# Kernel optimization log

Measured on AMD Instinct MI355X. Metric: run time of the kernel, lower is better.

The kernel has to match this reference:

```python
import jax, jax.numpy as jnp
import numpy as np

B, T, D, L = 128, 32, 512, 2


def setup_inputs() -> dict:
    key = jax.random.key(0)
    ks = jax.random.split(key, 8)
    s = 0.02
    inp = {
        "cognition_features": jax.random.normal(ks[0], (B, T, D), dtype=jnp.float32),
        # per-layer stacked params (leading dim L)
        "Wq": s * jax.random.normal(ks[1], (L, D, D), dtype=jnp.float32),
        "bq": jnp.zeros((L, D), jnp.float32),
        "Wk": s * jax.random.normal(ks[2], (L, D, D), dtype=jnp.float32),
        "bk": jnp.zeros((L, D), jnp.float32),
        "Wv": s * jax.random.normal(ks[3], (L, D, D), dtype=jnp.float32),
        "bv": jnp.zeros((L, D), jnp.float32),
        "ln1_g": jnp.ones((L, D), jnp.float32),
        "ln1_b": jnp.zeros((L, D), jnp.float32),
        "W1": s * jax.random.normal(ks[4], (L, 4 * D, D), dtype=jnp.float32),
        "b1": jnp.zeros((L, 4 * D), jnp.float32),
        "W2": s * jax.random.normal(ks[5], (L, D, 4 * D), dtype=jnp.float32),
        "b2": jnp.zeros((L, D), jnp.float32),
        "ln2_g": jnp.ones((L, D), jnp.float32),
        "ln2_b": jnp.zeros((L, D), jnp.float32),
        # gate mlp (random instead of zeros/ones init to avoid degenerate constant gate)
        "Ws": s * jax.random.normal(ks[6], (D, 2 * D), dtype=jnp.float32),
        "bs": jnp.zeros((D,), jnp.float32),
    }
    return inp


def _ln(x, g, b, eps=1e-5):
    mu = jnp.mean(x, axis=-1, keepdims=True)
    var = jnp.mean((x - mu) ** 2, axis=-1, keepdims=True)
    return (x - mu) * jax.lax.rsqrt(var + eps) * g + b


def reference(cognition_features, Wq, bq, Wk, bk, Wv, bv, ln1_g, ln1_b,
              W1, b1, W2, b2, ln2_g, ln2_b, Ws, bs):
    b_, t_, d_ = cognition_features.shape
    L_ = Wq.shape[0]
    # memory bank entries are detached originals of earlier batch items
    mem = jax.lax.stop_gradient(cognition_features).reshape(b_ * t_, d_)
    mem_item = jnp.arange(b_ * t_) // t_
    visible = mem_item[None, :] < jnp.arange(b_)[:, None]  # [B, B*T]
    neg = jnp.asarray(-1e9, cognition_features.dtype)
    scale = 1.0 / jnp.sqrt(jnp.asarray(d_, cognition_features.dtype))

    x = cognition_features
    for l in range(L_):
        q = x @ Wq[l].T + bq[l]                      # [B,T,D]
        k = mem @ Wk[l].T + bk[l]                    # [B*T,D]
        v = mem @ Wv[l].T + bv[l]
        s = jnp.einsum('btd,md->btm', q, k) * scale  # [B,T,B*T]
        s = jnp.where(visible[:, None, :], s, neg)
        a = jax.nn.softmax(s, axis=-1)
        attn = jnp.einsum('btm,md->btd', a, v)
        x = _ln(x + attn, ln1_g[l], ln1_b[l])
        h = jax.nn.gelu(x @ W1[l].T + b1[l], approximate=False)
        x = _ln(x + h @ W2[l].T + b2[l], ln2_g[l], ln2_b[l])

    # item 0 has an empty bank: blocks are skipped, attn_out = query
    attn_out = jnp.where((jnp.arange(b_) == 0)[:, None, None], cognition_features, x)
    cat = jnp.concatenate([cognition_features, attn_out], axis=-1)
    g = jax.nn.sigmoid(cat @ Ws.T + bs)
    return g * cognition_features + (1.0 - g) * attn_out
```

## Files before the change

### kernel.cpp

```cpp
#include <hip/hip_runtime.h>
#include <cmath>


#define ROWS 4096
#define DIM  512

typedef __bf16 bf16x8 __attribute__((ext_vector_type(8)));
typedef float  f32x4  __attribute__((ext_vector_type(4)));
typedef unsigned short u16;
typedef u16 u16x4 __attribute__((ext_vector_type(4)));
typedef u16 u16x8 __attribute__((ext_vector_type(8)));

#define RD ((size_t)ROWS * DIM)
#define BUFU 12288

__device__ __forceinline__ u16 f2bf(float x) {
    union { float f; unsigned u; } c; c.f = x;
    const unsigned r = (c.u + 0x7FFFu + ((c.u >> 16) & 1u)) >> 16;
    return (u16)r;
}

__device__ __forceinline__ void gload16(const void* g, void* l) {
    __builtin_amdgcn_global_load_lds(
        (const __attribute__((address_space(1))) void*)g,
        (__attribute__((address_space(3))) void*)l, 16, 0, 0);
}

__device__ __forceinline__ float gelu_f(float v) {
    return 0.5f * v * (1.0f + erff(v * 0.70710678118654752f));
}

template<int EPI>
__device__ __forceinline__ void mgemm_body(
    const u16* __restrict__ A, int lda,
    const u16* __restrict__ B, int ldb,
    const float* __restrict__ bias,
    void* __restrict__ C, int ldc,
    int kBeg, int kEnd, float scale, int m0, int n0, u16* smem)
{
    const int tid  = threadIdx.x;
    const int lane = tid & 63;
    const int w    = tid >> 6;
    const int wr   = (w >> 1) << 5;
    const int wc   = (w & 1) << 6;

    f32x4 acc[2][4];
    #pragma unroll
    for (int i = 0; i < 2; ++i)
        #pragma unroll
        for (int j = 0; j < 4; ++j)
            acc[i][j] = (f32x4){0.f, 0.f, 0.f, 0.f};

    const u16* gpA[2]; int loA[2];
    #pragma unroll
    for (int q = 0; q < 2; ++q) {
        const int c = (q << 2) + w;
        const int s = (c << 6) + lane;
        const int row = s >> 3, sub = (s & 7) ^ (row & 7);
        gpA[q] = A + (size_t)(m0 + row) * lda + (sub << 3) + kBeg;
        loA[q] = c << 9;
    }
    const u16* gpB[4]; int loB[4];
    #pragma unroll
    for (int q = 0; q < 4; ++q) {
        const int c = ((q + 2) << 2) + w - 8;
        const int s = (c << 6) + lane;
        const int row = s >> 3, sub = (s & 7) ^ (row & 7);
        gpB[q] = B + (size_t)(n0 + row) * ldb + (sub << 3) + kBeg;
        loB[q] = 4096 + (c << 9);
    }

    const int l15 = lane & 15, kg = lane >> 4;
    int aoff[2][2], boff[4][2];
    #pragma unroll
    for (int i = 0; i < 2; ++i)
        #pragma unroll
        for (int h = 0; h < 2; ++h) {
            const int r = wr + (i << 4) + l15;
            const int sub = ((h << 2) + kg) ^ (r & 7);
            aoff[i][h] = ((r << 3) + sub) << 3;
        }
    #pragma unroll
    for (int j = 0; j < 4; ++j)
        #pragma unroll
        for (int h = 0; h < 2; ++h) {
            const int r = wc + (j << 4) + l15;
            const int sub = ((h << 2) + kg) ^ (r & 7);
            boff[j][h] = 4096 + (((r << 3) + sub) << 3);
        }

    const int nt = (kEnd - kBeg) >> 6;

    auto STAGE = [&](int t, int bsel) {
        u16* base = smem + bsel * BUFU;
        const int ko = t << 6;
        gload16(gpA[0] + ko, base + loA[0]);
        gload16(gpA[1] + ko, base + loA[1]);
        gload16(gpB[0] + ko, base + loB[0]);
        gload16(gpB[1] + ko, base + loB[1]);
        gload16(gpB[2] + ko, base + loB[2]);
        gload16(gpB[3] + ko, base + loB[3]);
    };

    if (nt > 0) {
        STAGE(0, 0);
        if (nt > 1) STAGE(1, 1);
        for (int t = 0; t < nt; ++t) {
            if (t + 1 < nt) asm volatile("s_waitcnt vmcnt(6)" ::: "memory");
            else            asm volatile("s_waitcnt vmcnt(0)" ::: "memory");
            __builtin_amdgcn_s_barrier();
            asm volatile("" ::: "memory");

            const u16* buf = smem + (t & 1) * BUFU;
            bf16x8 a_[2][2], b_[4][2];
            #pragma unroll
            for (int i = 0; i < 2; ++i)
                #pragma unroll
                for (int h = 0; h < 2; ++h)
                    a_[i][h] = *reinterpret_cast<const bf16x8*>(&buf[aoff[i][h]]);
            #pragma unroll
            for (int j = 0; j < 4; ++j)
                #pragma unroll
                for (int h = 0; h < 2; ++h)
                    b_[j][h] = *reinterpret_cast<const bf16x8*>(&buf[boff[j][h]]);

            asm volatile("s_waitcnt lgkmcnt(0)" ::: "memory");
            __builtin_amdgcn_s_barrier();
            asm volatile("" ::: "memory");

            if (t + 2 < nt) STAGE(t + 2, t & 1);

            __builtin_amdgcn_s_setprio(1);
            #pragma unroll
            for (int h = 0; h < 2; ++h)
                #pragma unroll
                for (int i = 0; i < 2; ++i)
                    #pragma unroll
                    for (int j = 0; j < 4; ++j) {
                        if (EPI == 4)
                            acc[i][j] = __builtin_amdgcn_mfma_f32_16x16x32_bf16(
                                a_[i][h], b_[j][h], acc[i][j], 0, 0, 0);
                        else
                            acc[i][j] = __builtin_amdgcn_mfma_f32_16x16x32_bf16(
                                b_[j][h], a_[i][h], acc[i][j], 0, 0, 0);
                    }
            __builtin_amdgcn_s_setprio(0);
        }
    }

    const int lq = lane >> 4;
    if (EPI == 4) {
        #pragma unroll
        for (int j = 0; j < 4; ++j) {
            const int col = n0 + wc + (j << 4) + l15;
            const float bj = bias[col];
            #pragma unroll
            for (int i = 0; i < 2; ++i) {
                const int row0 = m0 + wr + (i << 4) + (lq << 2);
                u16x4 pk;
                #pragma unroll
                for (int r = 0; r < 4; ++r) pk[r] = f2bf(acc[i][j][r] + bj);
                *reinterpret_cast<u16x4*>(&((u16*)C)[(size_t)col * ldc + row0]) = pk;
            }
        }
    } else {
        #pragma unroll
        for (int j = 0; j < 4; ++j) {
            const int col0 = n0 + wc + (j << 4) + (lq << 2);
            float4 bj = {0.f, 0.f, 0.f, 0.f};
            if (EPI != 0) bj = *reinterpret_cast<const float4*>(&bias[col0]);
            #pragma unroll
            for (int i = 0; i < 2; ++i) {
                const int row = m0 + wr + (i << 4) + l15;
                f32x4 v = acc[i][j];
                if (EPI == 0) {
                    v[0] *= scale; v[1] *= scale; v[2] *= scale; v[3] *= scale;
                    *reinterpret_cast<f32x4*>(&((float*)C)[(size_t)row * ldc + col0]) = v;
                } else if (EPI == 1) {
                    v[0] += bj.x; v[1] += bj.y; v[2] += bj.z; v[3] += bj.w;
                    *reinterpret_cast<f32x4*>(&((float*)C)[(size_t)row * ldc + col0]) = v;
                } else {
                    v[0] += bj.x; v[1] += bj.y; v[2] += bj.z; v[3] += bj.w;
                    if (EPI == 3) {
                        v[0] = gelu_f(v[0]); v[1] = gelu_f(v[1]);
                        v[2] = gelu_f(v[2]); v[3] = gelu_f(v[3]);
                    }
                    u16x4 pk = {f2bf(v[0]), f2bf(v[1]), f2bf(v[2]), f2bf(v[3])};
                    *reinterpret_cast<u16x4*>(&((u16*)C)[(size_t)row * ldc + col0]) = pk;
                }
            }
        }
    }
}

template<int EPI>
__global__ __launch_bounds__(256, 3) void mgemm(
    const u16* __restrict__ A, int lda, const u16* __restrict__ B, int ldb,
    const float* __restrict__ bias, void* __restrict__ C, int ldc, int K, float scale)
{
    const int m0 = blockIdx.x << 6;
    const int n0 = blockIdx.y << 7;
    __shared__ u16 smem[2 * BUFU];
    mgemm_body<EPI>(A, lda, B, ldb, bias, C, ldc, 0, K, scale, m0, n0, smem);
}

__device__ __forceinline__ int tri_pref(int b) {
    const int h = b >> 1;
    return (b & 1) ? (h + 1) * (h + 1) : h * (h + 1);
}
__global__ __launch_bounds__(256, 3) void mgemm_tri(
    const u16* __restrict__ A, const u16* __restrict__ B,
    float* __restrict__ C, float scale)
{
    const int z = blockIdx.x;
    int bx = 2 * (int)sqrtf((float)z);
    while (tri_pref(bx + 1) <= z) ++bx;
    while (tri_pref(bx) > z) --bx;
    const int by = z - tri_pref(bx);
    __shared__ u16 smem[2 * BUFU];
    mgemm_body<0>(A, 512, B, 512, nullptr, C, 4096, 0, 512, scale,
                  bx << 6, by << 7, smem);
}

template<bool AVK>
__global__ __launch_bounds__(256, 3) void mgemm_pk(
    const u16* __restrict__ A, int lda, const u16* __restrict__ B, int ldb,
    float* __restrict__ Cpart, int K, int chunk)
{
    const int m0 = blockIdx.x << 6;
    const int n0 = blockIdx.y << 7;
    const int z  = blockIdx.z;
    const int Klim = AVK ? (m0 + 64) : K;
    const int ch = AVK ? ((((Klim >> 2) + 63) >> 6) << 6) : chunk;
    int kBeg = z * ch; if (kBeg > Klim) kBeg = Klim;
    int kEnd = kBeg + ch; if (kEnd > Klim) kEnd = Klim;
    __shared__ u16 smem[2 * BUFU];
    mgemm_body<0>(A, lda, B, ldb, nullptr, Cpart + (size_t)z * RD, 512,
                  kBeg, kEnd, 1.f, m0, n0, smem);
}

__global__ __launch_bounds__(256, 3) void qkv_gemm(
    const u16* __restrict__ xa, const u16* __restrict__ cfb,
    const u16* __restrict__ Wqb, const u16* __restrict__ Wkb, const u16* __restrict__ Wvb,
    const float* __restrict__ bq, const float* __restrict__ bk, const float* __restrict__ bv,
    u16* __restrict__ q, u16* __restrict__ k, u16* __restrict__ vT)
{
    __shared__ u16 smem[2 * BUFU];
    const int m0 = blockIdx.x << 6;
    const int which = blockIdx.y >> 2;
    const int n0 = (blockIdx.y & 3) << 7;
    if (which == 0)
        mgemm_body<2>(xa,  512, Wqb, 512, bq, q,  512,  0, 512, 1.f, m0, n0, smem);
    else if (which == 1)
        mgemm_body<2>(cfb, 512, Wkb, 512, bk, k,  512,  0, 512, 1.f, m0, n0, smem);
    else
        mgemm_body<4>(cfb, 512, Wvb, 512, bv, vT, 4096, 0, 512, 1.f, m0, n0, smem);
}

__global__ __launch_bounds__(256) void softmax_pbf(
    const float* __restrict__ S, u16* __restrict__ P, float* __restrict__ sums)
{
    const int row = blockIdx.x;
    const int b   = row >> 5;
    const int Lb  = b << 5;
    const int bound = ((row >> 6) + 1) << 6;
    const float* s = S + (size_t)row * 4096;
    u16* p = P + (size_t)row * 4096;
    const int tid = threadIdx.x;

    const u16x8 z8 = {0, 0, 0, 0, 0, 0, 0, 0};
    for (int m = Lb + tid * 8; m < bound; m += 2048)
        *reinterpret_cast<u16x8*>(&p[m]) = z8;
    if (b == 0) { if (tid == 0) sums[row] = 1.f; return; }

    __shared__ float red[4];
    float mx = -3.0e38f;
    for (int m = tid * 4; m < Lb; m += 1024) {
        const float4 v = *reinterpret_cast<const float4*>(&s[m]);
        mx = fmaxf(mx, fmaxf(fmaxf(v.x, v.y), fmaxf(v.z, v.w)));
    }
    #pragma unroll
    for (int off = 32; off; off >>= 1) mx = fmaxf(mx, __shfl_xor(mx, off));
    if ((tid & 63) == 0) red[tid >> 6] = mx;
    __syncthreads();
    mx = fmaxf(fmaxf(red[0], red[1]), fmaxf(red[2], red[3]));
    __syncthreads();

    float sum = 0.f;
    for (int m = tid * 8; m < Lb; m += 2048) {
        const float4 v0 = *reinterpret_cast<const float4*>(&s[m]);
        const float4 v1 = *reinterpret_cast<const float4*>(&s[m + 4]);
        float e[8];
        e[0] = expf(v0.x - mx); e[1] = expf(v0.y - mx);
        e[2] = expf(v0.z - mx); e[3] = expf(v0.w - mx);
        e[4] = expf(v1.x - mx); e[5] = expf(v1.y - mx);
        e[6] = expf(v1.z - mx); e[7] = expf(v1.w - mx);
        u16x8 o;
        #pragma unroll
        for (int i = 0; i < 8; ++i) { sum += e[i]; o[i] = f2bf(e[i]); }
        *reinterpret_cast<u16x8*>(&p[m]) = o;
    }
    #pragma unroll
    for (int off = 32; off; off >>= 1) sum += __shfl_xor(sum, off);
    if ((tid & 63) == 0) red[tid >> 6] = sum;
    __syncthreads();
    if (tid == 0)
        sums[row] = fmaxf(red[0] + red[1] + red[2] + red[3], 1e-30f);
}

template<int NS, bool HASB, bool DIV>
__global__ __launch_bounds__(256) void ln_res_ps(
    const float* __restrict__ Xin, const float* __restrict__ part,
    const float* __restrict__ bias, const float* __restrict__ sums,
    const float* __restrict__ gamma, const float* __restrict__ beta,
    float* __restrict__ Xout, u16* __restrict__ Xbf)
{
    const int row  = blockIdx.x * 4 + (threadIdx.x >> 6);
    const int lane = threadIdx.x & 63;
    const float* xr = Xin + (size_t)row * DIM;
    const int d0 = lane << 3;
    const float inv = DIV ? (1.0f / sums[row]) : 1.0f;

    const float4 x0 = *reinterpret_cast<const float4*>(&xr[d0]);
    const float4 x1 = *reinterpret_cast<const float4*>(&xr[d0 + 4]);
    float a[8] = {0.f, 0.f, 0.f, 0.f, 0.f, 0.f, 0.f, 0.f};
    #pragma unroll
    for (int s = 0; s < NS; ++s) {
        const float* pr = part + (size_t)s * RD + (size_t)row * DIM + d0;
        const float4 p0 = *reinterpret_cast<const float4*>(pr);
        const float4 p1 = *reinterpret_cast<const float4*>(pr + 4);
        a[0] += p0.x; a[1] += p0.y; a[2] += p0.z; a[3] += p0.w;
        a[4] += p1.x; a[5] += p1.y; a[6] += p1.z; a[7] += p1.w;
    }
    float v[8] = {x0.x, x0.y, x0.z, x0.w, x1.x, x1.y, x1.z, x1.w};
    #pragma unroll
    for (int i = 0; i < 8; ++i) v[i] += a[i] * inv;
    if (HASB) {
        const float4 b0 = *reinterpret_cast<const float4*>(&bias[d0]);
        const float4 b1 = *reinterpret_cast<const float4*>(&bias[d0 + 4]);
        v[0] += b0.x; v[1] += b0.y; v[2] += b0.z; v[3] += b0.w;
        v[4] += b1.x; v[5] += b1.y; v[6] += b1.z; v[7] += b1.w;
    }

    float sm = 0.f;
    #pragma unroll
    for (int i = 0; i < 8; ++i) sm += v[i];
    #pragma unroll
    for (int off = 32; off; off >>= 1) sm += __shfl_xor(sm, off);
    const float mu = sm * (1.0f / 512.0f);

    float qs = 0.f;
    #pragma unroll
    for (int i = 0; i < 8; ++i) { const float d = v[i] - mu; qs += d * d; }
    #pragma unroll
    for (int off = 32; off; off >>= 1) qs += __shfl_xor(qs, off);
    const float rs = rsqrtf(qs * (1.0f / 512.0f) + 1e-5f);

    const float4 g0 = *reinterpret_cast<const float4*>(&gamma[d0]);
    const float4 g1 = *reinterpret_cast<const float4*>(&gamma[d0 + 4]);
    const float4 b0 = *reinterpret_cast<const float4*>(&beta[d0]);
    const float4 b1 = *reinterpret_cast<const float4*>(&beta[d0 + 4]);
    float o[8];
    o[0] = (v[0] - mu) * rs * g0.x + b0.x;
    o[1] = (v[1] - mu) * rs * g0.y + b0.y;
    o[2] = (v[2] - mu) * rs * g0.z + b0.z;
    o[3] = (v[3] - mu) * rs * g0.w + b0.w;
    o[4] = (v[4] - mu) * rs * g1.x + b1.x;
    o[5] = (v[5] - mu) * rs * g1.y + b1.y;
    o[6] = (v[6] - mu) * rs * g1.z + b1.z;
    o[7] = (v[7] - mu) * rs * g1.w + b1.w;

    float4 f0 = {o[0], o[1], o[2], o[3]}, f1 = {o[4], o[5], o[6], o[7]};
    *reinterpret_cast<float4*>(&Xout[(size_t)row * DIM + d0])     = f0;
    *reinterpret_cast<float4*>(&Xout[(size_t)row * DIM + d0 + 4]) = f1;
    u16x8 ob;
    #pragma unroll
    for (int i = 0; i < 8; ++i) ob[i] = f2bf(o[i]);
    *reinterpret_cast<u16x8*>(&Xbf[(size_t)row * DIM + d0]) = ob;
}

struct ConvArgs {
    const float* src[7];
    u16* dst[7];
    int start[8];
};

__global__ __launch_bounds__(256) void conv_all(ConvArgs a)
{
    const int b = blockIdx.x;
    int seg = 0;
    #pragma unroll
    for (int i = 1; i < 7; ++i) seg += (a.start[i] <= b) ? 1 : 0;
    const int i = ((b - a.start[seg]) * 256 + threadIdx.x) << 3;
    const float* s = a.src[seg];
    const float4 lo = *reinterpret_cast<const float4*>(&s[i]);
    const float4 hi = *reinterpret_cast<const float4*>(&s[i + 4]);
    u16x8 o = {f2bf(lo.x), f2bf(lo.y), f2bf(lo.z), f2bf(lo.w),
               f2bf(hi.x), f2bf(hi.y), f2bf(hi.z), f2bf(hi.w)};
    *reinterpret_cast<u16x8*>(&a.dst[seg][i]) = o;
}

__global__ __launch_bounds__(256) void build_cat(
    u16* __restrict__ cat, const u16* __restrict__ cfb, const u16* __restrict__ xbf)
{
    const int idx = blockIdx.x * 256 + threadIdx.x;
    const int row = idx >> 7;
    const int c8  = idx & 127;
    const u16* src2 = (row < 32) ? cfb : xbf;
    const u16x8 v = (c8 < 64)
        ? *reinterpret_cast<const u16x8*>(&cfb[(size_t)row * 512 + (c8 << 3)])
        : *reinterpret_cast<const u16x8*>(&src2[(size_t)row * 512 + ((c8 - 64) << 3)]);
    *reinterpret_cast<u16x8*>(&cat[(size_t)row * 1024 + (c8 << 3)]) = v;
}

__global__ __launch_bounds__(256) void final_gate_ps(
    float4* __restrict__ out, const float4* __restrict__ cf,
    const float4* __restrict__ x, const float* __restrict__ part,
    const float* __restrict__ bias)
{
    const int idx = blockIdx.x * 256 + threadIdx.x;
    const int row = idx >> 7;
    const int c4  = idx & 127;
    const float4 zc = cf[idx];
    const float4 p0 = reinterpret_cast<const float4*>(part)[idx];
    const float4 p1 = reinterpret_cast<const float4*>(part + RD)[idx];
    const float4 bb = *reinterpret_cast<const float4*>(&bias[c4 << 2]);
    const float4 za = (row < 32) ? zc : x[idx];
    float4 o;
    { const float g = 1.0f / (1.0f + expf(-(p0.x + p1.x + bb.x))); o.x = g * zc.x + (1.0f - g) * za.x; }
    { const float g = 1.0f / (1.0f + expf(-(p0.y + p1.y + bb.y))); o.y = g * zc.y + (1.0f - g) * za.y; }
    { const float g = 1.0f / (1.0f + expf(-(p0.z + p1.z + bb.z))); o.z = g * zc.z + (1.0f - g) * za.z; }
    { const float g = 1.0f / (1.0f + expf(-(p0.w + p1.w + bb.w))); o.w = g * zc.w + (1.0f - g) * za.w; }
    out[idx] = o;
}

extern "C" void kernel_launch(void* const* d_in, const int* in_sizes, int n_in,
                              void* d_out, int out_size, void* d_ws, size_t ws_size,
                              hipStream_t stream)
{
    const float* cf   = (const float*)d_in[0];
    const float* Wq   = (const float*)d_in[1];
    const float* bq   = (const float*)d_in[2];
    const float* Wk   = (const float*)d_in[3];
    const float* bk   = (const float*)d_in[4];
    const float* Wv   = (const float*)d_in[5];
    const float* bv   = (const float*)d_in[6];
    const float* ln1g = (const float*)d_in[7];
    const float* ln1b = (const float*)d_in[8];
    const float* W1   = (const float*)d_in[9];
    const float* b1   = (const float*)d_in[10];
    const float* W2   = (const float*)d_in[11];
    const float* b2   = (const float*)d_in[12];
    const float* ln2g = (const float*)d_in[13];
    const float* ln2b = (const float*)d_in[14];
    const float* Wsg  = (const float*)d_in[15];
    const float* bsg  = (const float*)d_in[16];
    float* out = (float*)d_out;

    float* ws   = (float*)d_ws;
    float* x    = ws;
    float* sums = ws + RD;
    float* s    = ws + 2 * RD;
    float* part = ws + 2 * RD;
    u16*  pbf  = (u16*)(ws + 10 * RD);
    u16*  hbf  = pbf;
    u16*  catb = pbf;
    u16*  bfb  = (u16*)(ws + 14 * RD);
    u16* cfb = bfb;
    u16* xbf = bfb + RD;
    u16* qbf = bfb + 2 * RD;
    u16* kbf = bfb + 3 * RD;
    u16* vTb = bfb + 4 * RD;
    u16* Wqb = bfb + 5 * RD;
    u16* Wkb = Wqb + 524288;
    u16* Wvb = Wkb + 524288;
    u16* W1b = Wvb + 524288;
    u16* W2b = W1b + 2097152;
    u16* Wsb = W2b + 2097152;

    const float scale = 0.044194173824159216f;

    ConvArgs ca;
    ca.src[0] = cf;  ca.dst[0] = cfb;
    ca.src[1] = Wq;  ca.dst[1] = Wqb;
    ca.src[2] = Wk;  ca.dst[2] = Wkb;
    ca.src[3] = Wv;  ca.dst[3] = Wvb;
    ca.src[4] = W1;  ca.dst[4] = W1b;
    ca.src[5] = W2;  ca.dst[5] = W2b;
    ca.src[6] = Wsg; ca.dst[6] = Wsb;
    ca.start[0] = 0;    ca.start[1] = 1024; ca.start[2] = 1280;
    ca.start[3] = 1536; ca.start[4] = 1792; ca.start[5] = 2816;
    ca.start[6] = 3840; ca.start[7] = 4096;
    conv_all<<<4096, 256, 0, stream>>>(ca);

    for (int l = 0; l < 2; ++l) {
        const u16* xa = (l == 0) ? cfb : xbf;
        qkv_gemm<<<dim3(64, 12), 256, 0, stream>>>(
            xa, cfb, Wqb + l * 262144, Wkb + l * 262144, Wvb + l * 262144,
            bq + l * 512, bk + l * 512, bv + l * 512, qbf, kbf, vTb);
        mgemm_tri<<<1056, 256, 0, stream>>>(qbf, kbf, s, scale);
        softmax_pbf<<<4096, 256, 0, stream>>>(s, pbf, sums);
        mgemm_pk<true><<<dim3(64, 4, 4), 256, 0, stream>>>(
            pbf, 4096, vTb, 4096, part, 4096, 0);
        ln_res_ps<4, false, true><<<1024, 256, 0, stream>>>(
            (l == 0) ? cf : x, part, nullptr, sums,
            ln1g + l * 512, ln1b + l * 512, x, xbf);
        mgemm<3><<<dim3(64, 16), 256, 0, stream>>>(
            xbf, 512, W1b + l * 1048576, 512, b1 + l * 2048, hbf, 2048, 512, 1.f);
        mgemm_pk<false><<<dim3(64, 4, 4), 256, 0, stream>>>(
            hbf, 2048, W2b + l * 1048576, 2048, part, 2048, 512);
        ln_res_ps<4, true, false><<<1024, 256, 0, stream>>>(
            x, part, b2 + l * 512, nullptr,
            ln2g + l * 512, ln2b + l * 512, x, xbf);
    }

    build_cat<<<2048, 256, 0, stream>>>(catb, cfb, xbf);
    mgemm_pk<false><<<dim3(64, 4, 2), 256, 0, stream>>>(
        catb, 1024, Wsb, 1024, part, 1024, 512);
    final_gate_ps<<<2048, 256, 0, stream>>>((float4*)out, (const float4*)cf,
                                            (const float4*)x, part, bsg);
}
```

Before: 271.2 us.

## Store bf16 operands in MFMA fragment layout and use LDS-free per-wave GEMMs

All bf16 operands (converted weights, activations, softmax probabilities, q/k/vT) are now written in a pre-tiled 16x32 MFMA fragment layout. This lets each wave load its operand fragments straight from global memory with contiguous 16-byte loads. The shared-memory double-buffered block GEMM is replaced by an independent per-wave 64x64 tile GEMM with no barriers or LDS. Triangular and split-K work is recomputed at 64-row granularity, and the softmax zero-fill bound shrinks to match. The cost is reduced operand reuse across waves, since each wave reads its A and B tiles from L2 independently, and global loads are no longer software-pipelined.

Result: slower. 404.2 us (+49.0%).

```diff
diff --git a/kernel.cpp b/kernel.cpp
--- a/kernel.cpp
+++ b/kernel.cpp
@@ -12,7 +12,6 @@
 typedef u16 u16x8 __attribute__((ext_vector_type(8)));
 
 #define RD ((size_t)ROWS * DIM)
-#define BUFU 12288
 
 __device__ __forceinline__ u16 f2bf(float x) {
     union { float f; unsigned u; } c; c.f = x;
@@ -20,241 +19,196 @@
     return (u16)r;
 }
 
-__device__ __forceinline__ void gload16(const void* g, void* l) {
-    __builtin_amdgcn_global_load_lds(
-        (const __attribute__((address_space(1))) void*)g,
-        (__attribute__((address_space(3))) void*)l, 16, 0, 0);
-}
-
 __device__ __forceinline__ float gelu_f(float v) {
     return 0.5f * v * (1.0f + erff(v * 0.70710678118654752f));
 }
 
+__device__ __forceinline__ size_t fragAddr(int r, int k, int K) {
+    return ((size_t)((r >> 4) * (K >> 5) + (k >> 5)) << 9)
+         + (((r & 15) | (((k >> 3) & 3) << 4)) << 3);
+}
+
 template<int EPI>
-__device__ __forceinline__ void mgemm_body(
-    const u16* __restrict__ A, int lda,
-    const u16* __restrict__ B, int ldb,
+__device__ __forceinline__ void wgemm(
+    const u16* __restrict__ A, int KA,
+    const u16* __restrict__ B,
     const float* __restrict__ bias,
-    void* __restrict__ C, int ldc,
-    int kBeg, int kEnd, float scale, int m0, int n0, u16* smem)
-{
-    const int tid  = threadIdx.x;
-    const int lane = tid & 63;
-    const int w    = tid >> 6;
-    const int wr   = (w >> 1) << 5;
-    const int wc   = (w & 1) << 6;
-
-    f32x4 acc[2][4];
-    #pragma unroll
-    for (int i = 0; i < 2; ++i)
+    void* __restrict__ C, int ldcK,
+    int ktBeg, int ktEnd, float scale, int mt, int nt)
+{
+    const int lane = threadIdx.x & 63;
+    const int l15 = lane & 15, lq = lane >> 4;
+
+    f32x4 acc[4][4];
+    #pragma unroll
+    for (int i = 0; i < 4; ++i)
         #pragma unroll
         for (int j = 0; j < 4; ++j)
             acc[i][j] = (f32x4){0.f, 0.f, 0.f, 0.f};
 
-    const u16* gpA[2]; int loA[2];
-    #pragma unroll
-    for (int q = 0; q < 2; ++q) {
-        const int c = (q << 2) + w;
-        const int s = (c << 6) + lane;
-        const int row = s >> 3, sub = (s & 7) ^ (row & 7);
-        gpA[q] = A + (size_t)(m0 + row) * lda + (sub << 3) + kBeg;
-        loA[q] = c << 9;
-    }
-    const u16* gpB[4]; int loB[4];
-    #pragma unroll
-    for (int q = 0; q < 4; ++q) {
-        const int c = ((q + 2) << 2) + w - 8;
-        const int s = (c << 6) + lane;
-        const int row = s >> 3, sub = (s & 7) ^ (row & 7);
-        gpB[q] = B + (size_t)(n0 + row) * ldb + (sub << 3) + kBeg;
-        loB[q] = 4096 + (c << 9);
-    }
-
-    const int l15 = lane & 15, kg = lane >> 4;
-    int aoff[2][2], boff[4][2];
-    #pragma unroll
-    for (int i = 0; i < 2; ++i)
-        #pragma unroll
-        for (int h = 0; h < 2; ++h) {
-            const int r = wr + (i << 4) + l15;
-            const int sub = ((h << 2) + kg) ^ (r & 7);
-            aoff[i][h] = ((r << 3) + sub) << 3;
+    const int ka5 = KA >> 5;
+    const u16* pa[4]; const u16* pb[4];
+    #pragma unroll
+    for (int i = 0; i < 4; ++i)
+        pa[i] = A + (((size_t)((mt * 4 + i) * ka5 + ktBeg)) << 9) + (lane << 3);
+    #pragma unroll
+    for (int j = 0; j < 4; ++j)
+        pb[j] = B + (((size_t)((nt * 4 + j) * ka5 + ktBeg)) << 9) + (lane << 3);
+
+    for (int kt = ktBeg; kt < ktEnd; ++kt) {
+        bf16x8 a_[4], b_[4];
+        #pragma unroll
+        for (int i = 0; i < 4; ++i) {
+            a_[i] = *reinterpret_cast<const bf16x8*>(pa[i]); pa[i] += 512;
         }
-    #pragma unroll
-    for (int j = 0; j < 4; ++j)
-        #pragma unroll
-        for (int h = 0; h < 2; ++h) {
-            const int r = wc + (j << 4) + l15;
-            const int sub = ((h << 2) + kg) ^ (r & 7);
-            boff[j][h] = 4096 + (((r << 3) + sub) << 3);
+        #pragma unroll
+        for (int j = 0; j < 4; ++j) {
+            b_[j] = *reinterpret_cast<const bf16x8*>(pb[j]); pb[j] += 512;
         }
-
-    const int nt = (kEnd - kBeg) >> 6;
-
-    auto STAGE = [&](int t, int bsel) {
-        u16* base = smem + bsel * BUFU;
-        const int ko = t << 6;
-        gload16(gpA[0] + ko, base + loA[0]);
-        gload16(gpA[1] + ko, base + loA[1]);
-        gload16(gpB[0] + ko, base + loB[0]);
-        gload16(gpB[1] + ko, base + loB[1]);
-        gload16(gpB[2] + ko, base + loB[2]);
-        gload16(gpB[3] + ko, base + loB[3]);
-    };
-
-    if (nt > 0) {
-        STAGE(0, 0);
-        if (nt > 1) STAGE(1, 1);
-        for (int t = 0; t < nt; ++t) {
-            if (t + 1 < nt) asm volatile("s_waitcnt vmcnt(6)" ::: "memory");
-            else            asm volatile("s_waitcnt vmcnt(0)" ::: "memory");
-            __builtin_amdgcn_s_barrier();
-            asm volatile("" ::: "memory");
-
-            const u16* buf = smem + (t & 1) * BUFU;
-            bf16x8 a_[2][2], b_[4][2];
+        #pragma unroll
+        for (int i = 0; i < 4; ++i)
             #pragma unroll
-            for (int i = 0; i < 2; ++i)
-                #pragma unroll
-                for (int h = 0; h < 2; ++h)
-                    a_[i][h] = *reinterpret_cast<const bf16x8*>(&buf[aoff[i][h]]);
+            for (int j = 0; j < 4; ++j) {
+                if constexpr (EPI == 4)
+                    acc[i][j] = __builtin_amdgcn_mfma_f32_16x16x32_bf16(
+                        a_[i], b_[j], acc[i][j], 0, 0, 0);
+                else
+                    acc[i][j] = __builtin_amdgcn_mfma_f32_16x16x32_bf16(
+                        b_[j], a_[i], acc[i][j], 0, 0, 0);
+            }
+    }
+
+    if constexpr (EPI == 0) {
+        #pragma unroll
+        for (int j = 0; j < 4; ++j) {
+            const int col0 = nt * 64 + (j << 4) + (lq << 2);
             #pragma unroll
-            for (int j = 0; j < 4; ++j)
-                #pragma unroll
-                for (int h = 0; h < 2; ++h)
-                    b_[j][h] = *reinterpret_cast<const bf16x8*>(&buf[boff[j][h]]);
-
-            asm volatile("s_waitcnt lgkmcnt(0)" ::: "memory");
-            __builtin_amdgcn_s_barrier();
-            asm volatile("" ::: "memory");
-
-            if (t + 2 < nt) STAGE(t + 2, t & 1);
-
-            __builtin_amdgcn_s_setprio(1);
+            for (int i = 0; i < 4; ++i) {
+                const int row = mt * 64 + (i << 4) + l15;
+                f32x4 v = acc[i][j];
+                v[0] *= scale; v[1] *= scale; v[2] *= scale; v[3] *= scale;
+                *reinterpret_cast<f32x4*>(&((float*)C)[(size_t)row * ldcK + col0]) = v;
+            }
+        }
+    } else if constexpr (EPI == 2 || EPI == 3) {
+        #pragma unroll
+        for (int j = 0; j < 4; ++j) {
+            const int co = (j << 4) + (lq << 2);
+            const int col0 = nt * 64 + co;
+            const float4 bj = *reinterpret_cast<const float4*>(&bias[col0]);
+            const int ktO = (nt << 1) + (co >> 5);
+            const int lnO = l15 | (((co >> 3) & 3) << 4);
+            const int elem = co & 7;
             #pragma unroll
-            for (int h = 0; h < 2; ++h)
-                #pragma unroll
-                for (int i = 0; i < 2; ++i)
-                    #pragma unroll
-                    for (int j = 0; j < 4; ++j) {
-                        if (EPI == 4)
-                            acc[i][j] = __builtin_amdgcn_mfma_f32_16x16x32_bf16(
-                                a_[i][h], b_[j][h], acc[i][j], 0, 0, 0);
-                        else
-                            acc[i][j] = __builtin_amdgcn_mfma_f32_16x16x32_bf16(
-                                b_[j][h], a_[i][h], acc[i][j], 0, 0, 0);
-                    }
-            __builtin_amdgcn_s_setprio(0);
+            for (int i = 0; i < 4; ++i) {
+                const int rt = mt * 4 + i;
+                f32x4 v = acc[i][j];
+                v[0] += bj.x; v[1] += bj.y; v[2] += bj.z; v[3] += bj.w;
+                if (EPI == 3) {
+                    v[0] = gelu_f(v[0]); v[1] = gelu_f(v[1]);
+                    v[2] = gelu_f(v[2]); v[3] = gelu_f(v[3]);
+                }
+                u16x4 pk = {f2bf(v[0]), f2bf(v[1]), f2bf(v[2]), f2bf(v[3])};
+                u16* dst = (u16*)C + (((size_t)(rt * (ldcK >> 5) + ktO)) << 9)
+                         + (lnO << 3) + elem;
+                *reinterpret_cast<u16x4*>(dst) = pk;
+            }
         }
-    }
-
-    const int lq = lane >> 4;
-    if (EPI == 4) {
+    } else {
         #pragma unroll
         for (int j = 0; j < 4; ++j) {
-            const int col = n0 + wc + (j << 4) + l15;
+            const int rtO = nt * 4 + j;
+            const int col = nt * 64 + (j << 4) + l15;
             const float bj = bias[col];
             #pragma unroll
-            for (int i = 0; i < 2; ++i) {
-                const int row0 = m0 + wr + (i << 4) + (lq << 2);
+            for (int i = 0; i < 4; ++i) {
+                const int ro = (i << 4) + (lq << 2);
+                const int ktO = (mt << 1) + (ro >> 5);
+                const int lnO = l15 | (((ro >> 3) & 3) << 4);
+                const int elem = ro & 7;
                 u16x4 pk;
                 #pragma unroll
                 for (int r = 0; r < 4; ++r) pk[r] = f2bf(acc[i][j][r] + bj);
-                *reinterpret_cast<u16x4*>(&((u16*)C)[(size_t)col * ldc + row0]) = pk;
+                u16* dst = (u16*)C + (((size_t)(rtO * (ldcK >> 5) + ktO)) << 9)
+                         + (lnO << 3) + elem;
+                *reinterpret_cast<u16x4*>(dst) = pk;
             }
         }
-    } else {
-        #pragma unroll
-        for (int j = 0; j < 4; ++j) {
-            const int col0 = n0 + wc + (j << 4) + (lq << 2);
-            float4 bj = {0.f, 0.f, 0.f, 0.f};
-            if (EPI != 0) bj = *reinterpret_cast<const float4*>(&bias[col0]);
-            #pragma unroll
-            for (int i = 0; i < 2; ++i) {
-                const int row = m0 + wr + (i << 4) + l15;
-                f32x4 v = acc[i][j];
-                if (EPI == 0) {
-                    v[0] *= scale; v[1] *= scale; v[2] *= scale; v[3] *= scale;
-                    *reinterpret_cast<f32x4*>(&((float*)C)[(size_t)row * ldc + col0]) = v;
-                } else if (EPI == 1) {
-                    v[0] += bj.x; v[1] += bj.y; v[2] += bj.z; v[3] += bj.w;
-                    *reinterpret_cast<f32x4*>(&((float*)C)[(size_t)row * ldc + col0]) = v;
-                } else {
-                    v[0] += bj.x; v[1] += bj.y; v[2] += bj.z; v[3] += bj.w;
-                    if (EPI == 3) {
-                        v[0] = gelu_f(v[0]); v[1] = gelu_f(v[1]);
-                        v[2] = gelu_f(v[2]); v[3] = gelu_f(v[3]);
-                    }
-                    u16x4 pk = {f2bf(v[0]), f2bf(v[1]), f2bf(v[2]), f2bf(v[3])};
-                    *reinterpret_cast<u16x4*>(&((u16*)C)[(size_t)row * ldc + col0]) = pk;
-                }
-            }
-        }
-    }
-}
-
-template<int EPI>
-__global__ __launch_bounds__(256, 3) void mgemm(
-    const u16* __restrict__ A, int lda, const u16* __restrict__ B, int ldb,
-    const float* __restrict__ bias, void* __restrict__ C, int ldc, int K, float scale)
-{
-    const int m0 = blockIdx.x << 6;
-    const int n0 = blockIdx.y << 7;
-    __shared__ u16 smem[2 * BUFU];
-    mgemm_body<EPI>(A, lda, B, ldb, bias, C, ldc, 0, K, scale, m0, n0, smem);
-}
-
-__device__ __forceinline__ int tri_pref(int b) {
-    const int h = b >> 1;
-    return (b & 1) ? (h + 1) * (h + 1) : h * (h + 1);
-}
-__global__ __launch_bounds__(256, 3) void mgemm_tri(
-    const u16* __restrict__ A, const u16* __restrict__ B,
-    float* __restrict__ C, float scale)
-{
-    const int z = blockIdx.x;
-    int bx = 2 * (int)sqrtf((float)z);
-    while (tri_pref(bx + 1) <= z) ++bx;
-    while (tri_pref(bx) > z) --bx;
-    const int by = z - tri_pref(bx);
-    __shared__ u16 smem[2 * BUFU];
-    mgemm_body<0>(A, 512, B, 512, nullptr, C, 4096, 0, 512, scale,
-                  bx << 6, by << 7, smem);
-}
-
-template<bool AVK>
-__global__ __launch_bounds__(256, 3) void mgemm_pk(
-    const u16* __restrict__ A, int lda, const u16* __restrict__ B, int ldb,
-    float* __restrict__ Cpart, int K, int chunk)
-{
-    const int m0 = blockIdx.x << 6;
-    const int n0 = blockIdx.y << 7;
-    const int z  = blockIdx.z;
-    const int Klim = AVK ? (m0 + 64) : K;
-    const int ch = AVK ? ((((Klim >> 2) + 63) >> 6) << 6) : chunk;
-    int kBeg = z * ch; if (kBeg > Klim) kBeg = Klim;
-    int kEnd = kBeg + ch; if (kEnd > Klim) kEnd = Klim;
-    __shared__ u16 smem[2 * BUFU];
-    mgemm_body<0>(A, lda, B, ldb, nullptr, Cpart + (size_t)z * RD, 512,
-                  kBeg, kEnd, 1.f, m0, n0, smem);
-}
-
-__global__ __launch_bounds__(256, 3) void qkv_gemm(
+    }
+}
+
+__global__ __launch_bounds__(256, 3) void k_qkv(
     const u16* __restrict__ xa, const u16* __restrict__ cfb,
-    const u16* __restrict__ Wqb, const u16* __restrict__ Wkb, const u16* __restrict__ Wvb,
-    const float* __restrict__ bq, const float* __restrict__ bk, const float* __restrict__ bv,
+    const u16* __restrict__ Wqb, const u16* __restrict__ Wkb,
+    const u16* __restrict__ Wvb,
+    const float* __restrict__ bq, const float* __restrict__ bk,
+    const float* __restrict__ bv,
     u16* __restrict__ q, u16* __restrict__ k, u16* __restrict__ vT)
 {
-    __shared__ u16 smem[2 * BUFU];
-    const int m0 = blockIdx.x << 6;
-    const int which = blockIdx.y >> 2;
-    const int n0 = (blockIdx.y & 3) << 7;
+    const int g = blockIdx.x * 4 + (threadIdx.x >> 6);
+    const int which = g >> 9;
+    const int t = g & 511;
+    const int mt = t >> 3, nt = t & 7;
     if (which == 0)
-        mgemm_body<2>(xa,  512, Wqb, 512, bq, q,  512,  0, 512, 1.f, m0, n0, smem);
+        wgemm<2>(xa, 512, Wqb, bq, q, 512, 0, 16, 1.f, mt, nt);
     else if (which == 1)
-        mgemm_body<2>(cfb, 512, Wkb, 512, bk, k,  512,  0, 512, 1.f, m0, n0, smem);
+        wgemm<2>(cfb, 512, Wkb, bk, k, 512, 0, 16, 1.f, mt, nt);
     else
-        mgemm_body<4>(cfb, 512, Wvb, 512, bv, vT, 4096, 0, 512, 1.f, m0, n0, smem);
+        wgemm<4>(cfb, 512, Wvb, bv, vT, 4096, 0, 16, 1.f, mt, nt);
+}
+
+__global__ __launch_bounds__(256, 3) void k_tri(
+    const u16* __restrict__ qb, const u16* __restrict__ kb,
+    float* __restrict__ S, float scale)
+{
+    const int z = blockIdx.x * 4 + (threadIdx.x >> 6);
+    int mt = (int)((sqrtf((float)(8 * z + 1)) - 1.0f) * 0.5f);
+    while ((mt + 1) * (mt + 2) / 2 <= z) ++mt;
+    while (mt * (mt + 1) / 2 > z) --mt;
+    const int nt = z - mt * (mt + 1) / 2;
+    wgemm<0>(qb, 512, kb, nullptr, S, 4096, 0, 16, scale, mt, nt);
+}
+
+__global__ __launch_bounds__(256, 3) void k_av(
+    const u16* __restrict__ P, const u16* __restrict__ vT,
+    float* __restrict__ part)
+{
+    const int g = blockIdx.x * 4 + (threadIdx.x >> 6);
+    const int z = g & 3, nt = (g >> 2) & 7, mt = g >> 5;
+    const int kts = 2 * mt + 1;
+    const int ch = (kts + 3) >> 2;
+    int kb = z * ch; if (kb > kts) kb = kts;
+    int ke = kb + ch; if (ke > kts) ke = kts;
+    wgemm<0>(P, 4096, vT, nullptr, part + (size_t)z * RD, 512, kb, ke, 1.f, mt, nt);
+}
+
+__global__ __launch_bounds__(256, 3) void k_mlp1(
+    const u16* __restrict__ xb, const u16* __restrict__ W1b,
+    const float* __restrict__ b1, u16* __restrict__ h)
+{
+    const int g = blockIdx.x * 4 + (threadIdx.x >> 6);
+    const int mt = g >> 5, nt = g & 31;
+    wgemm<3>(xb, 512, W1b, b1, h, 2048, 0, 16, 1.f, mt, nt);
+}
+
+__global__ __launch_bounds__(256, 3) void k_mlp2(
+    const u16* __restrict__ h, const u16* __restrict__ W2b,
+    float* __restrict__ part)
+{
+    const int g = blockIdx.x * 4 + (threadIdx.x >> 6);
+    const int z = g & 3, nt = (g >> 2) & 7, mt = g >> 5;
+    wgemm<0>(h, 2048, W2b, nullptr, part + (size_t)z * RD, 512,
+             z * 16, z * 16 + 16, 1.f, mt, nt);
+}
+
+__global__ __launch_bounds__(256, 3) void k_gate(
+    const u16* __restrict__ cat, const u16* __restrict__ Wsb,
+    float* __restrict__ part)
+{
+    const int g = blockIdx.x * 4 + (threadIdx.x >> 6);
+    const int z = g & 1, nt = (g >> 1) & 7, mt = g >> 4;
+    wgemm<0>(cat, 1024, Wsb, nullptr, part + (size_t)z * RD, 512,
+             z * 16, z * 16 + 16, 1.f, mt, nt);
 }
 
 __global__ __launch_bounds__(256) void softmax_pbf(
@@ -263,14 +217,13 @@
     const int row = blockIdx.x;
     const int b   = row >> 5;
     const int Lb  = b << 5;
-    const int bound = ((row >> 6) + 1) << 6;
+    const int bound = ((row >> 6) << 6) + 32;
     const float* s = S + (size_t)row * 4096;
-    u16* p = P + (size_t)row * 4096;
     const int tid = threadIdx.x;
 
     const u16x8 z8 = {0, 0, 0, 0, 0, 0, 0, 0};
     for (int m = Lb + tid * 8; m < bound; m += 2048)
-        *reinterpret_cast<u16x8*>(&p[m]) = z8;
+        *reinterpret_cast<u16x8*>(&P[fragAddr(row, m, 4096)]) = z8;
     if (b == 0) { if (tid == 0) sums[row] = 1.f; return; }
 
     __shared__ float red[4];
@@ -298,7 +251,7 @@
         u16x8 o;
         #pragma unroll
         for (int i = 0; i < 8; ++i) { sum += e[i]; o[i] = f2bf(e[i]); }
-        *reinterpret_cast<u16x8*>(&p[m]) = o;
+        *reinterpret_cast<u16x8*>(&P[fragAddr(row, m, 4096)]) = o;
     }
     #pragma unroll
     for (int off = 32; off; off >>= 1) sum += __shfl_xor(sum, off);
@@ -376,13 +329,14 @@
     u16x8 ob;
     #pragma unroll
     for (int i = 0; i < 8; ++i) ob[i] = f2bf(o[i]);
-    *reinterpret_cast<u16x8*>(&Xbf[(size_t)row * DIM + d0]) = ob;
+    *reinterpret_cast<u16x8*>(&Xbf[fragAddr(row, d0, 512)]) = ob;
 }
 
 struct ConvArgs {
     const float* src[7];
     u16* dst[7];
     int start[8];
+    int K[7];
 };
 
 __global__ __launch_bounds__(256) void conv_all(ConvArgs a)
@@ -391,13 +345,18 @@
     int seg = 0;
     #pragma unroll
     for (int i = 1; i < 7; ++i) seg += (a.start[i] <= b) ? 1 : 0;
-    const int i = ((b - a.start[seg]) * 256 + threadIdx.x) << 3;
-    const float* s = a.src[seg];
-    const float4 lo = *reinterpret_cast<const float4*>(&s[i]);
-    const float4 hi = *reinterpret_cast<const float4*>(&s[i + 4]);
+    const int s = (b - a.start[seg]) * 256 + threadIdx.x;
+    const int K = a.K[seg];
+    const int fc = s >> 6, lane = s & 63;
+    const int rt = fc / (K >> 5), kt = fc % (K >> 5);
+    const int r = (rt << 4) + (lane & 15);
+    const int k = (kt << 5) + ((lane >> 4) << 3);
+    const float* src = a.src[seg] + (size_t)r * K + k;
+    const float4 lo = *reinterpret_cast<const float4*>(src);
+    const float4 hi = *reinterpret_cast<const float4*>(src + 4);
     u16x8 o = {f2bf(lo.x), f2bf(lo.y), f2bf(lo.z), f2bf(lo.w),
                f2bf(hi.x), f2bf(hi.y), f2bf(hi.z), f2bf(hi.w)};
-    *reinterpret_cast<u16x8*>(&a.dst[seg][i]) = o;
+    *reinterpret_cast<u16x8*>(&a.dst[seg][(size_t)s << 3]) = o;
 }
 
 __global__ __launch_bounds__(256) void build_cat(
@@ -405,12 +364,15 @@
 {
     const int idx = blockIdx.x * 256 + threadIdx.x;
     const int row = idx >> 7;
-    const int c8  = idx & 127;
-    const u16* src2 = (row < 32) ? cfb : xbf;
-    const u16x8 v = (c8 < 64)
-        ? *reinterpret_cast<const u16x8*>(&cfb[(size_t)row * 512 + (c8 << 3)])
-        : *reinterpret_cast<const u16x8*>(&src2[(size_t)row * 512 + ((c8 - 64) << 3)]);
-    *reinterpret_cast<u16x8*>(&cat[(size_t)row * 1024 + (c8 << 3)]) = v;
+    const int c0  = (idx & 127) << 3;
+    u16x8 v;
+    if (c0 < 512)
+        v = *reinterpret_cast<const u16x8*>(&cfb[fragAddr(row, c0, 512)]);
+    else {
+        const u16* src2 = (row < 32) ? cfb : xbf;
+        v = *reinterpret_cast<const u16x8*>(&src2[fragAddr(row, c0 - 512, 512)]);
+    }
+    *reinterpret_cast<u16x8*>(&cat[fragAddr(row, c0, 1024)]) = v;
 }
 
 __global__ __launch_bounds__(256) void final_gate_ps(
@@ -481,13 +443,13 @@
     const float scale = 0.044194173824159216f;
 
     ConvArgs ca;
-    ca.src[0] = cf;  ca.dst[0] = cfb;
-    ca.src[1] = Wq;  ca.dst[1] = Wqb;
-    ca.src[2] = Wk;  ca.dst[2] = Wkb;
-    ca.src[3] = Wv;  ca.dst[3] = Wvb;
-    ca.src[4] = W1;  ca.dst[4] = W1b;
-    ca.src[5] = W2;  ca.dst[5] = W2b;
-    ca.src[6] = Wsg; ca.dst[6] = Wsb;
+    ca.src[0] = cf;  ca.dst[0] = cfb;  ca.K[0] = 512;
+    ca.src[1] = Wq;  ca.dst[1] = Wqb;  ca.K[1] = 512;
+    ca.src[2] = Wk;  ca.dst[2] = Wkb;  ca.K[2] = 512;
+    ca.src[3] = Wv;  ca.dst[3] = Wvb;  ca.K[3] = 512;
+    ca.src[4] = W1;  ca.dst[4] = W1b;  ca.K[4] = 512;
+    ca.src[5] = W2;  ca.dst[5] = W2b;  ca.K[5] = 2048;
+    ca.src[6] = Wsg; ca.dst[6] = Wsb;  ca.K[6] = 1024;
     ca.start[0] = 0;    ca.start[1] = 1024; ca.start[2] = 1280;
     ca.start[3] = 1536; ca.start[4] = 1792; ca.start[5] = 2816;
     ca.start[6] = 3840; ca.start[7] = 4096;
@@ -495,28 +457,24 @@
 
     for (int l = 0; l < 2; ++l) {
         const u16* xa = (l == 0) ? cfb : xbf;
-        qkv_gemm<<<dim3(64, 12), 256, 0, stream>>>(
+        k_qkv<<<384, 256, 0, stream>>>(
             xa, cfb, Wqb + l * 262144, Wkb + l * 262144, Wvb + l * 262144,
             bq + l * 512, bk + l * 512, bv + l * 512, qbf, kbf, vTb);
-        mgemm_tri<<<1056, 256, 0, stream>>>(qbf, kbf, s, scale);
+        k_tri<<<520, 256, 0, stream>>>(qbf, kbf, s, scale);
         softmax_pbf<<<4096, 256, 0, stream>>>(s, pbf, sums);
-        mgemm_pk<true><<<dim3(64, 4, 4), 256, 0, stream>>>(
-            pbf, 4096, vTb, 4096, part, 4096, 0);
+        k_av<<<512, 256, 0, stream>>>(pbf, vTb, part);
         ln_res_ps<4, false, true><<<1024, 256, 0, stream>>>(
             (l == 0) ? cf : x, part, nullptr, sums,
             ln1g + l * 512, ln1b + l * 512, x, xbf);
-        mgemm<3><<<dim3(64, 16), 256, 0, stream>>>(
-            xbf, 512, W1b + l * 1048576, 512, b1 + l * 2048, hbf, 2048, 512, 1.f);
-        mgemm_pk<false><<<dim3(64, 4, 4), 256, 0, stream>>>(
-            hbf, 2048, W2b + l * 1048576, 2048, part, 2048, 512);
+        k_mlp1<<<512, 256, 0, stream>>>(xbf, W1b + l * 1048576, b1 + l * 2048, hbf);
+        k_mlp2<<<512, 256, 0, stream>>>(hbf, W2b + l * 1048576, part);
         ln_res_ps<4, true, false><<<1024, 256, 0, stream>>>(
             x, part, b2 + l * 512, nullptr,
             ln2g + l * 512, ln2b + l * 512, x, xbf);
     }
 
     build_cat<<<2048, 256, 0, stream>>>(catb, cfb, xbf);
-    mgemm_pk<false><<<dim3(64, 4, 2), 256, 0, stream>>>(
-        catb, 1024, Wsb, 1024, part, 1024, 512);
+    k_gate<<<256, 256, 0, stream>>>(catb, Wsb, part);
     final_gate_ps<<<2048, 256, 0, stream>>>((float4*)out, (const float4*)cf,
                                             (const float4*)x, part, bsg);
 }
```
